# Performance work log

Hardware: AMD Instinct MI355X
Metric: run time of the kernel (lower is better)

Reference implementation:

```python
import jax, jax.numpy as jnp
import numpy as np

DIM = 1024
ATT_DIM = 1024
N_HEADS = 16
HEAD_DIM = ATT_DIM // N_HEADS


def q_rsqrt_np(x):
    # Quake fast inverse sqrt with one Newton iteration, as in the source.
    y = np.asarray([x], dtype=np.float32)
    x2 = y * np.float32(0.5)
    i = y.view(np.int32)
    i = np.right_shift(i, 1)
    i = np.int32(1597463007) - i
    y = i.view(np.float32)
    y = y * (np.float32(1.5) - x2 * y * y)
    # module casts to half: self.scaling = q_rsqrt(head_dim).half()
    return float(np.float16(y[0]))

SCALING = q_rsqrt_np(HEAD_DIM)


def own_softmax(x):
    # max in fp32, exp in fp32, cast exp to fp16, sum in fp16, divide -> fp16
    maxes = jnp.max(x, axis=-1, keepdims=True)
    x_exp = jnp.exp(x - maxes).astype(jnp.float16)
    x_exp_sum = jnp.sum(x_exp, axis=-1, keepdims=True)
    return x_exp / x_exp_sum


def setup_inputs() -> dict:
    key = jax.random.key(0)
    k1, k2, k3 = jax.random.split(key, 3)
    tgt_len = 2048
    x = jax.random.normal(k1, (tgt_len, DIM), dtype=jnp.float32)
    # nn.Linear weights: [out_features, in_features]
    W_in = jax.random.normal(k2, (3 * ATT_DIM, DIM), dtype=jnp.float32) * (1.0 / np.sqrt(DIM))
    W_out = jax.random.normal(k3, (DIM, ATT_DIM), dtype=jnp.float32) * (1.0 / np.sqrt(ATT_DIM))
    return {"x": x, "W_in": W_in, "W_out": W_out, "tgt_len": tgt_len}


def reference(x, W_in, W_out, tgt_len):
    qkv = x @ W_in.T  # [N, 3*att_dim]
    q, k, v = jnp.split(qkv, 3, axis=-1)
    # [N, H, D] -> [H, N, D]
    q = q.reshape(tgt_len, N_HEADS, HEAD_DIM).transpose(1, 0, 2)
    k = k.reshape(tgt_len, N_HEADS, HEAD_DIM).transpose(1, 0, 2)
    v = v.reshape(tgt_len, N_HEADS, HEAD_DIM).transpose(1, 0, 2)
    scores = jnp.einsum('hnd,hmd->hnm', q, k) * SCALING  # [H, N, N] fp32
    probs = own_softmax(scores)  # fp16
    ctx = jnp.einsum('hnm,hmd->hnd', probs.astype(jnp.float32), v)  # [H, N, D]
    ctx = ctx.transpose(1, 0, 2).reshape(tgt_len, ATT_DIM)
    return ctx @ W_out.T
```

## Files before the change

kernel.cpp:

```cpp
#include <hip/hip_runtime.h>
#include <cstring>
#include <cstdint>

#define TGT 2048
#define NH 16
#define HD 64
#define DIM 1024
#define OD3 3072

typedef _Float16 f16x8 __attribute__((ext_vector_type(8)));
typedef _Float16 f16x4 __attribute__((ext_vector_type(4)));
typedef _Float16 f16x2 __attribute__((ext_vector_type(2)));
typedef float f32x4 __attribute__((ext_vector_type(4)));

__device__ __forceinline__ void gload16(const void* g, void* l) {
  __builtin_amdgcn_global_load_lds(
      (const __attribute__((address_space(1))) unsigned int*)g,
      (__attribute__((address_space(3))) unsigned int*)l, 16, 0, 0);
}

__global__ void cast_all(const float* __restrict__ x, const float* __restrict__ win,
                         const float* __restrict__ wout, _Float16* __restrict__ xh,
                         _Float16* __restrict__ winh, _Float16* __restrict__ wouth) {
  const int NX = TGT * DIM / 8, NW = OD3 * DIM / 8, NO = DIM * DIM / 8;
  int i = blockIdx.x * blockDim.x + threadIdx.x;
  const float* src;
  _Float16* dst;
  int off;
  if (i < NX) { src = x; dst = xh; off = i; }
  else if (i < NX + NW) { src = win; dst = winh; off = i - NX; }
  else if (i < NX + NW + NO) { src = wout; dst = wouth; off = i - NX - NW; }
  else return;
  const float4* p = (const float4*)(src + (size_t)off * 8);
  float4 a = p[0], b = p[1];
  f16x8 o;
  o[0] = (_Float16)a.x; o[1] = (_Float16)a.y; o[2] = (_Float16)a.z; o[3] = (_Float16)a.w;
  o[4] = (_Float16)b.x; o[5] = (_Float16)b.y; o[6] = (_Float16)b.z; o[7] = (_Float16)b.w;
  *(f16x8*)(dst + (size_t)off * 8) = o;
}

__global__ __launch_bounds__(256, 3) void gemm_qkv(
    const _Float16* __restrict__ A, const _Float16* __restrict__ B,
    _Float16* __restrict__ qh, _Float16* __restrict__ kg, _Float16* __restrict__ vg) {
  __shared__ __attribute__((aligned(16))) _Float16 As[2][2048];
  __shared__ __attribute__((aligned(16))) _Float16 Bs[2][4096];
  const int tid = threadIdx.x, lane = tid & 63, w = tid >> 6;
  const int g = lane >> 4, c = lane & 15;
  const int wr = w >> 1, wc = w & 1;
  const int id = blockIdx.x;
  const int xcd = id & 7, r = id >> 3;
  const int mh = xcd & 1, nq = xcd >> 1;
  const int bm = mh * 1024 + (r / 6) * 64;
  const int bn = nq * 768 + (r % 6) * 128;
  f32x4 acc[2][4] = {};

#define QKV_STAGE(buf, k0)                                                              \
  {                                                                                     \
    gload16(A + (size_t)(bm + (tid & 63)) * DIM + (k0) + (tid >> 6) * 8,                \
            &As[buf][tid * 8]);                                                         \
    _Pragma("unroll") for (int t = 0; t < 2; ++t) {                                     \
      int e = t * 256 + tid;                                                            \
      gload16(B + (size_t)(bn + (e & 127)) * DIM + (k0) + (e >> 7) * 8,                 \
              &Bs[buf][e * 8]);                                                         \
    }                                                                                   \
  }

  QKV_STAGE(0, 0);
  __syncthreads();
  for (int kk = 0; kk < 32; ++kk) {
    const int cur = kk & 1;
    if (kk + 1 < 32) QKV_STAGE(cur ^ 1, (kk + 1) * 32);
    f16x8 af[2], bf[4];
#pragma unroll
    for (int m = 0; m < 2; ++m) af[m] = *(const f16x8*)(&As[cur][g * 512 + (wr * 32 + m * 16 + c) * 8]);
#pragma unroll
    for (int n = 0; n < 4; ++n) bf[n] = *(const f16x8*)(&Bs[cur][g * 1024 + (wc * 64 + n * 16 + c) * 8]);
    __builtin_amdgcn_s_setprio(1);
#pragma unroll
    for (int m = 0; m < 2; ++m)
#pragma unroll
      for (int n = 0; n < 4; ++n)
        acc[m][n] = __builtin_amdgcn_mfma_f32_16x16x32_f16(af[m], bf[n], acc[m][n], 0, 0, 0);
    __builtin_amdgcn_s_setprio(0);
    __syncthreads();
  }
#undef QKV_STAGE

  const int which = bn >> 10;
  const int bnn = bn & 1023;
  if (which == 0) {
#pragma unroll
    for (int m = 0; m < 2; ++m)
#pragma unroll
      for (int n = 0; n < 4; ++n)
#pragma unroll
        for (int j = 0; j < 4; ++j) {
          int row = bm + wr * 32 + m * 16 + g * 4 + j;
          int o = bnn + wc * 64 + n * 16 + c;
          qh[((size_t)(o >> 6) * TGT + row) * HD + (o & 63)] = (_Float16)acc[m][n][j];
        }
  } else if (which == 1) {
#pragma unroll
    for (int m = 0; m < 2; ++m)
#pragma unroll
      for (int n = 0; n < 4; ++n)
#pragma unroll
        for (int j = 0; j < 4; ++j) {
          int krow = bm + wr * 32 + m * 16 + g * 4 + j;
          int o = bnn + wc * 64 + n * 16 + c;
          int hh = o >> 6, d = o & 63;
          int kt = krow >> 6, rr = krow & 63;
          int blk = (rr >> 4) * 2 + (d >> 5);
          int ln = (rr & 15) + 16 * ((d >> 3) & 3);
          kg[(size_t)hh * 131072 + kt * 4096 + (blk * 64 + ln) * 8 + (d & 7)] =
              (_Float16)acc[m][n][j];
        }
  } else {
#pragma unroll
    for (int m = 0; m < 2; ++m)
#pragma unroll
      for (int n = 0; n < 4; ++n) {
        int krow0 = bm + wr * 32 + m * 16 + g * 4;
        int o = bnn + wc * 64 + n * 16 + c;
        int hh = o >> 6, d = o & 63;
        int kt = krow0 >> 6, k = krow0 & 63;
        int np = d >> 4, cc = d & 15;
        int ks2 = k >> 5, gg = (k >> 2) & 3, e0 = 4 * ((k >> 4) & 1);
        f16x4 v;
#pragma unroll
        for (int j = 0; j < 4; ++j) v[j] = (_Float16)acc[m][n][j];
        *(f16x4*)(vg + (size_t)hh * 131072 + kt * 4096 +
                  ((np * 2 + ks2) * 64 + cc + 16 * gg) * 8 + e0) = v;
      }
  }
}

__global__ __launch_bounds__(256, 2) void gemm_out(
    const _Float16* __restrict__ A, const _Float16* __restrict__ B, float* __restrict__ out) {
  __shared__ __attribute__((aligned(16))) _Float16 As[2][2048];
  __shared__ __attribute__((aligned(16))) _Float16 Bs[2][2048];
  const int tid = threadIdx.x, lane = tid & 63, w = tid >> 6;
  const int g = lane >> 4, c = lane & 15;
  const int wr = w >> 1, wc = w & 1;
  const int id = blockIdx.x;
  const int xcd = id & 7, r = id >> 3;
  const int mh = xcd & 1, nq = xcd >> 1;
  const int bm = mh * 1024 + (r / 4) * 64;
  const int bn = nq * 256 + (r % 4) * 64;
  f32x4 acc[2][2] = {};

#define OUT_STAGE(buf, k0)                                                              \
  {                                                                                     \
    gload16(A + (size_t)(bm + (tid & 63)) * DIM + (k0) + (tid >> 6) * 8,                \
            &As[buf][tid * 8]);                                                         \
    gload16(B + (size_t)(bn + (tid & 63)) * DIM + (k0) + (tid >> 6) * 8,                \
            &Bs[buf][tid * 8]);                                                         \
  }

  OUT_STAGE(0, 0);
  __syncthreads();
  for (int kk = 0; kk < 32; ++kk) {
    const int cur = kk & 1;
    if (kk + 1 < 32) OUT_STAGE(cur ^ 1, (kk + 1) * 32);
    f16x8 af[2], bf[2];
#pragma unroll
    for (int m = 0; m < 2; ++m) af[m] = *(const f16x8*)(&As[cur][g * 512 + (wr * 32 + m * 16 + c) * 8]);
#pragma unroll
    for (int n = 0; n < 2; ++n) bf[n] = *(const f16x8*)(&Bs[cur][g * 512 + (wc * 32 + n * 16 + c) * 8]);
    __builtin_amdgcn_s_setprio(1);
#pragma unroll
    for (int m = 0; m < 2; ++m)
#pragma unroll
      for (int n = 0; n < 2; ++n)
        acc[m][n] = __builtin_amdgcn_mfma_f32_16x16x32_f16(af[m], bf[n], acc[m][n], 0, 0, 0);
    __builtin_amdgcn_s_setprio(0);
    __syncthreads();
  }
#undef OUT_STAGE

#pragma unroll
  for (int m = 0; m < 2; ++m)
#pragma unroll
    for (int n = 0; n < 2; ++n)
#pragma unroll
      for (int j = 0; j < 4; ++j) {
        int row = bm + wr * 32 + m * 16 + g * 4 + j;
        int o = bn + wc * 32 + n * 16 + c;
        out[(size_t)row * DIM + o] = acc[m][n][j];
      }
}

__global__ __launch_bounds__(512, 4) void attn(
    const _Float16* __restrict__ qh, const _Float16* __restrict__ kg,
    const _Float16* __restrict__ vg, _Float16* __restrict__ ctxh, float scal2) {
  __shared__ __attribute__((aligned(16))) _Float16 Ks[2][2][4096];
  __shared__ __attribute__((aligned(16))) _Float16 Vs[2][2][4096];
  const int tid = threadIdx.x;
  const int grp = tid >> 8, t256 = tid & 255;
  const int lane = tid & 63, w = (tid >> 6) & 3;
  const int g = lane >> 4, c = lane & 15;
  const int h = blockIdx.y, qblk = blockIdx.x;
  const int qrow = qblk * 64 + w * 16 + c;
  const _Float16* kb = kg + (size_t)h * 131072 + (size_t)grp * 65536;
  const _Float16* vb = vg + (size_t)h * 131072 + (size_t)grp * 65536;

  f16x8 qf[2];
#pragma unroll
  for (int ks = 0; ks < 2; ++ks)
    qf[ks] = *(const f16x8*)(qh + ((size_t)h * TGT + qrow) * HD + ks * 32 + g * 8);

  float m2 = -INFINITY, lsum = 0.f;
  f32x4 oacc[4] = {};

#define ATTN_STAGE(buf, kt)                                                         \
  {                                                                                 \
    _Pragma("unroll") for (int t = 0; t < 2; ++t) {                                 \
      int chunk = t * 256 + t256;                                                   \
      gload16(kb + (size_t)(kt) * 4096 + chunk * 8, &Ks[grp][buf][chunk * 8]);      \
      gload16(vb + (size_t)(kt) * 4096 + chunk * 8, &Vs[grp][buf][chunk * 8]);      \
    }                                                                               \
  }

  ATTN_STAGE(0, 0);
  __syncthreads();

  for (int kt = 0; kt < 16; ++kt) {
    const int cur = kt & 1;
    if (kt + 1 < 16) ATTN_STAGE(cur ^ 1, kt + 1);

    f32x4 s[4] = {};
    __builtin_amdgcn_s_setprio(1);
#pragma unroll
    for (int n = 0; n < 4; ++n)
#pragma unroll
      for (int ks = 0; ks < 2; ++ks) {
        f16x8 kf = *(const f16x8*)(&Ks[grp][cur][((n * 2 + ks) * 64 + lane) * 8]);
        s[n] = __builtin_amdgcn_mfma_f32_16x16x32_f16(kf, qf[ks], s[n], 0, 0, 0);
      }
    __builtin_amdgcn_s_setprio(0);

    f32x4 m4;
#pragma unroll
    for (int j = 0; j < 4; ++j) m4[j] = fmaxf(fmaxf(s[0][j], s[1][j]), fmaxf(s[2][j], s[3][j]));
    float mx = fmaxf(fmaxf(m4[0], m4[1]), fmaxf(m4[2], m4[3]));
    mx = fmaxf(mx, __shfl_xor(mx, 16));
    mx = fmaxf(mx, __shfl_xor(mx, 32));
    float pmax = mx * scal2;

    if (!__all(pmax <= m2 + 8.f)) {
      float mnew = fmaxf(m2, pmax);
      float alpha = __builtin_amdgcn_exp2f(m2 - mnew);
      m2 = mnew;
      lsum *= alpha;
#pragma unroll
      for (int np = 0; np < 4; ++np)
#pragma unroll
        for (int j = 0; j < 4; ++j) oacc[np][j] *= alpha;
    }

    float tsum = 0.f;
    uint32_t pk[4][2];
#pragma unroll
    for (int n = 0; n < 4; ++n) {
      float p0 = __builtin_amdgcn_exp2f(__builtin_fmaf(s[n][0], scal2, -m2));
      float p1 = __builtin_amdgcn_exp2f(__builtin_fmaf(s[n][1], scal2, -m2));
      float p2 = __builtin_amdgcn_exp2f(__builtin_fmaf(s[n][2], scal2, -m2));
      float p3 = __builtin_amdgcn_exp2f(__builtin_fmaf(s[n][3], scal2, -m2));
      tsum += (p0 + p1) + (p2 + p3);
      auto a = __builtin_amdgcn_cvt_pkrtz(p0, p1);
      auto b = __builtin_amdgcn_cvt_pkrtz(p2, p3);
      memcpy(&pk[n][0], &a, 4);
      memcpy(&pk[n][1], &b, 4);
    }
    tsum += __shfl_xor(tsum, 16);
    tsum += __shfl_xor(tsum, 32);
    lsum += tsum;

#pragma unroll
    for (int ks = 0; ks < 2; ++ks) {
      f16x8 pa;
      memcpy(&pa, &pk[2 * ks][0], 16);
      __builtin_amdgcn_s_setprio(1);
#pragma unroll
      for (int np = 0; np < 4; ++np) {
        f16x8 vbf = *(const f16x8*)(&Vs[grp][cur][((np * 2 + ks) * 64 + lane) * 8]);
        oacc[np] = __builtin_amdgcn_mfma_f32_16x16x32_f16(vbf, pa, oacc[np], 0, 0, 0);
      }
      __builtin_amdgcn_s_setprio(0);
    }
    __syncthreads();
  }
#undef ATTN_STAGE

  float* smo = (float*)&Ks[0][0][0];
  float* sml = (float*)&Vs[0][0][0];
  if (grp == 1) {
#pragma unroll
    for (int np = 0; np < 4; ++np)
#pragma unroll
      for (int j = 0; j < 4; ++j) smo[t256 * 16 + np * 4 + j] = oacc[np][j];
    sml[t256 * 2] = m2;
    sml[t256 * 2 + 1] = lsum;
  }
  __syncthreads();
  if (grp == 0) {
    float m1 = sml[t256 * 2], l1 = sml[t256 * 2 + 1];
    float mm = fmaxf(m2, m1);
    float e0 = __builtin_amdgcn_exp2f(m2 - mm);
    float e1 = __builtin_amdgcn_exp2f(m1 - mm);
    float inv = 1.0f / (lsum * e0 + l1 * e1);
#pragma unroll
    for (int np = 0; np < 4; ++np) {
      f16x4 o4;
#pragma unroll
      for (int j = 0; j < 4; ++j)
        o4[j] = (_Float16)((oacc[np][j] * e0 + smo[t256 * 16 + np * 4 + j] * e1) * inv);
      *(f16x4*)(ctxh + (size_t)qrow * DIM + h * HD + np * 16 + g * 4) = o4;
    }
  }
}

static float fp16_round_host(float x) {
  uint32_t u; memcpy(&u, &x, 4);
  uint32_t sign = u & 0x80000000u;
  uint32_t exp = (u >> 23) & 0xff;
  uint32_t m = u & 0x7fffffu;
  uint32_t low = m & 0x1fffu, hi = m >> 13;
  if (low > 0x1000u || (low == 0x1000u && (hi & 1))) hi++;
  if (hi == 0x400u) { hi = 0; exp++; }
  uint32_t r = sign | (exp << 23) | (hi << 13);
  float f; memcpy(&f, &r, 4); return f;
}

extern "C" void kernel_launch(void* const* d_in, const int* in_sizes, int n_in,
                              void* d_out, int out_size, void* d_ws, size_t ws_size,
                              hipStream_t stream) {
  const float* x = (const float*)d_in[0];
  const float* Win = (const float*)d_in[1];
  const float* Wout = (const float*)d_in[2];
  float* out = (float*)d_out;
  char* ws = (char*)d_ws;
  _Float16* xh    = (_Float16*)(ws);
  _Float16* winh  = (_Float16*)(ws + (4ull << 20));
  _Float16* wouth = (_Float16*)(ws + (10ull << 20));
  _Float16* qh    = (_Float16*)(ws + (12ull << 20));
  _Float16* kg    = (_Float16*)(ws + (16ull << 20));
  _Float16* vg    = (_Float16*)(ws + (20ull << 20));
  _Float16* ctxh  = (_Float16*)(ws + (24ull << 20));

  float y = 64.0f;
  volatile float x2 = 32.0f;
  int ib; memcpy(&ib, &y, 4);
  ib = 1597463007 - (ib >> 1);
  memcpy(&y, &ib, 4);
  volatile float t1 = x2 * y;
  volatile float t2 = t1 * y;
  volatile float t3 = 1.5f - t2;
  y = y * t3;
  const float scaling = fp16_round_host(y);
  const float scal2 = scaling * 1.4426950408889634f;

  const int ncast = (TGT * DIM + OD3 * DIM + DIM * DIM) / 8;
  cast_all<<<(ncast + 255) / 256, 256, 0, stream>>>(x, Win, Wout, xh, winh, wouth);
  gemm_qkv<<<768, 256, 0, stream>>>(xh, winh, qh, kg, vg);
  attn<<<dim3(32, NH), 512, 0, stream>>>(qh, kg, vg, ctxh, scal2);
  gemm_out<<<512, 256, 0, stream>>>(ctxh, wouth, out);
}
```

Baseline: 100.4 us.

## Load GEMM fragments directly from global into registers, dropping LDS staging

Both projection GEMMs (QKV and output) stop staging tiles through shared memory with global_load_lds and barriers. Each wave now loads its MFMA fragments straight from global memory into registers, double-buffered in registers, and occupancy hints rise to 4 blocks. This removes LDS traffic and __syncthreads. In exchange, waves that share a tile row or column load the same data redundantly and reads become less coalesced, leaning on L2/L1 caches.

```diff
diff --git a/kernel.cpp b/kernel.cpp
--- a/kernel.cpp
+++ b/kernel.cpp
@@ -39,11 +39,9 @@
   *(f16x8*)(dst + (size_t)off * 8) = o;
 }
 
-__global__ __launch_bounds__(256, 3) void gemm_qkv(
+__global__ __launch_bounds__(256, 4) void gemm_qkv(
     const _Float16* __restrict__ A, const _Float16* __restrict__ B,
     _Float16* __restrict__ qh, _Float16* __restrict__ kg, _Float16* __restrict__ vg) {
-  __shared__ __attribute__((aligned(16))) _Float16 As[2][2048];
-  __shared__ __attribute__((aligned(16))) _Float16 Bs[2][4096];
   const int tid = threadIdx.x, lane = tid & 63, w = tid >> 6;
   const int g = lane >> 4, c = lane & 15;
   const int wr = w >> 1, wc = w & 1;
@@ -52,39 +50,37 @@
   const int mh = xcd & 1, nq = xcd >> 1;
   const int bm = mh * 1024 + (r / 6) * 64;
   const int bn = nq * 768 + (r % 6) * 128;
+  const _Float16* Ab = A + (size_t)(bm + wr * 32 + c) * DIM + g * 8;
+  const _Float16* Bb = B + (size_t)(bn + wc * 64 + c) * DIM + g * 8;
   f32x4 acc[2][4] = {};
 
-#define QKV_STAGE(buf, k0)                                                              \
-  {                                                                                     \
-    gload16(A + (size_t)(bm + (tid & 63)) * DIM + (k0) + (tid >> 6) * 8,                \
-            &As[buf][tid * 8]);                                                         \
-    _Pragma("unroll") for (int t = 0; t < 2; ++t) {                                     \
-      int e = t * 256 + tid;                                                            \
-      gload16(B + (size_t)(bn + (e & 127)) * DIM + (k0) + (e >> 7) * 8,                 \
-              &Bs[buf][e * 8]);                                                         \
-    }                                                                                   \
-  }
-
-  QKV_STAGE(0, 0);
-  __syncthreads();
-  for (int kk = 0; kk < 32; ++kk) {
-    const int cur = kk & 1;
-    if (kk + 1 < 32) QKV_STAGE(cur ^ 1, (kk + 1) * 32);
-    f16x8 af[2], bf[4];
-#pragma unroll
-    for (int m = 0; m < 2; ++m) af[m] = *(const f16x8*)(&As[cur][g * 512 + (wr * 32 + m * 16 + c) * 8]);
-#pragma unroll
-    for (int n = 0; n < 4; ++n) bf[n] = *(const f16x8*)(&Bs[cur][g * 1024 + (wc * 64 + n * 16 + c) * 8]);
-    __builtin_amdgcn_s_setprio(1);
-#pragma unroll
-    for (int m = 0; m < 2; ++m)
-#pragma unroll
-      for (int n = 0; n < 4; ++n)
-        acc[m][n] = __builtin_amdgcn_mfma_f32_16x16x32_f16(af[m], bf[n], acc[m][n], 0, 0, 0);
-    __builtin_amdgcn_s_setprio(0);
-    __syncthreads();
-  }
-#undef QKV_STAGE
+#define QKV_LOAD(afv, bfv, kk)                                                      \
+  {                                                                                 \
+    _Pragma("unroll") for (int m = 0; m < 2; ++m)                                   \
+      afv[m] = *(const f16x8*)(Ab + (size_t)m * 16 * DIM + (kk) * 32);              \
+    _Pragma("unroll") for (int n = 0; n < 4; ++n)                                   \
+      bfv[n] = *(const f16x8*)(Bb + (size_t)n * 16 * DIM + (kk) * 32);              \
+  }
+#define QKV_MFMA(afv, bfv)                                                          \
+  {                                                                                 \
+    __builtin_amdgcn_s_setprio(1);                                                  \
+    _Pragma("unroll") for (int m = 0; m < 2; ++m)                                   \
+      _Pragma("unroll") for (int n = 0; n < 4; ++n)                                 \
+        acc[m][n] = __builtin_amdgcn_mfma_f32_16x16x32_f16(afv[m], bfv[n],          \
+                                                           acc[m][n], 0, 0, 0);    \
+    __builtin_amdgcn_s_setprio(0);                                                  \
+  }
+
+  f16x8 afa[2], bfa[4], afb[2], bfb[4];
+  QKV_LOAD(afa, bfa, 0);
+  for (int kk = 0; kk < 32; kk += 2) {
+    QKV_LOAD(afb, bfb, kk + 1);
+    QKV_MFMA(afa, bfa);
+    if (kk + 2 < 32) QKV_LOAD(afa, bfa, kk + 2);
+    QKV_MFMA(afb, bfb);
+  }
+#undef QKV_LOAD
+#undef QKV_MFMA
 
   const int which = bn >> 10;
   const int bnn = bn & 1023;
@@ -135,10 +131,8 @@
   }
 }
 
-__global__ __launch_bounds__(256, 2) void gemm_out(
+__global__ __launch_bounds__(256, 4) void gemm_out(
     const _Float16* __restrict__ A, const _Float16* __restrict__ B, float* __restrict__ out) {
-  __shared__ __attribute__((aligned(16))) _Float16 As[2][2048];
-  __shared__ __attribute__((aligned(16))) _Float16 Bs[2][2048];
   const int tid = threadIdx.x, lane = tid & 63, w = tid >> 6;
   const int g = lane >> 4, c = lane & 15;
   const int wr = w >> 1, wc = w & 1;
@@ -147,36 +141,37 @@
   const int mh = xcd & 1, nq = xcd >> 1;
   const int bm = mh * 1024 + (r / 4) * 64;
   const int bn = nq * 256 + (r % 4) * 64;
+  const _Float16* Ab = A + (size_t)(bm + wr * 32 + c) * DIM + g * 8;
+  const _Float16* Bb = B + (size_t)(bn + wc * 32 + c) * DIM + g * 8;
   f32x4 acc[2][2] = {};
 
-#define OUT_STAGE(buf, k0)                                                              \
-  {                                                                                     \
-    gload16(A + (size_t)(bm + (tid & 63)) * DIM + (k0) + (tid >> 6) * 8,                \
-            &As[buf][tid * 8]);                                                         \
-    gload16(B + (size_t)(bn + (tid & 63)) * DIM + (k0) + (tid >> 6) * 8,                \
-            &Bs[buf][tid * 8]);                                                         \
-  }
-
-  OUT_STAGE(0, 0);
-  __syncthreads();
-  for (int kk = 0; kk < 32; ++kk) {
-    const int cur = kk & 1;
-    if (kk + 1 < 32) OUT_STAGE(cur ^ 1, (kk + 1) * 32);
-    f16x8 af[2], bf[2];
-#pragma unroll
-    for (int m = 0; m < 2; ++m) af[m] = *(const f16x8*)(&As[cur][g * 512 + (wr * 32 + m * 16 + c) * 8]);
-#pragma unroll
-    for (int n = 0; n < 2; ++n) bf[n] = *(const f16x8*)(&Bs[cur][g * 512 + (wc * 32 + n * 16 + c) * 8]);
-    __builtin_amdgcn_s_setprio(1);
-#pragma unroll
-    for (int m = 0; m < 2; ++m)
-#pragma unroll
-      for (int n = 0; n < 2; ++n)
-        acc[m][n] = __builtin_amdgcn_mfma_f32_16x16x32_f16(af[m], bf[n], acc[m][n], 0, 0, 0);
-    __builtin_amdgcn_s_setprio(0);
-    __syncthreads();
-  }
-#undef OUT_STAGE
+#define OUT_LOAD(afv, bfv, kk)                                                      \
+  {                                                                                 \
+    _Pragma("unroll") for (int m = 0; m < 2; ++m)                                   \
+      afv[m] = *(const f16x8*)(Ab + (size_t)m * 16 * DIM + (kk) * 32);              \
+    _Pragma("unroll") for (int n = 0; n < 2; ++n)                                   \
+      bfv[n] = *(const f16x8*)(Bb + (size_t)n * 16 * DIM + (kk) * 32);              \
+  }
+#define OUT_MFMA(afv, bfv)                                                          \
+  {                                                                                 \
+    __builtin_amdgcn_s_setprio(1);                                                  \
+    _Pragma("unroll") for (int m = 0; m < 2; ++m)                                   \
+      _Pragma("unroll") for (int n = 0; n < 2; ++n)                                 \
+        acc[m][n] = __builtin_amdgcn_mfma_f32_16x16x32_f16(afv[m], bfv[n],          \
+                                                           acc[m][n], 0, 0, 0);    \
+    __builtin_amdgcn_s_setprio(0);                                                  \
+  }
+
+  f16x8 afa[2], bfa[2], afb[2], bfb[2];
+  OUT_LOAD(afa, bfa, 0);
+  for (int kk = 0; kk < 32; kk += 2) {
+    OUT_LOAD(afb, bfb, kk + 1);
+    OUT_MFMA(afa, bfa);
+    if (kk + 2 < 32) OUT_LOAD(afa, bfa, kk + 2);
+    OUT_MFMA(afb, bfb);
+  }
+#undef OUT_LOAD
+#undef OUT_MFMA
 
 #pragma unroll
   for (int m = 0; m < 2; ++m)
```

Result: slower. 138.7 us (+38.1%).
